# Performance work log

Measured on AMD Instinct MI355X. Metric: run time of the kernel, lower is better.

The kernel has to match this reference:

```python
import jax, jax.numpy as jnp
import numpy as np

B, D_IN, D_OUT, E = 8192, 1024, 1024, 16

def setup_inputs() -> dict:
    key = jax.random.key(0)
    k1, k2, k3 = jax.random.split(key, 3)
    scale_in = 1.0 / np.sqrt(D_IN)
    return {
        "x": jax.random.normal(k1, (B, D_IN), dtype=jnp.float32),
        "Wg": jax.random.normal(k2, (D_IN, E), dtype=jnp.float32) * scale_in,
        "bg": jnp.zeros((E,), dtype=jnp.float32),
        "We": jax.random.normal(k3, (E, D_IN, D_OUT), dtype=jnp.float32) * scale_in,
        "be": jnp.zeros((E, D_OUT), dtype=jnp.float32),
    }

def reference(x, Wg, bg, We, be):
    # gate: Linear + softmax over experts  -> [B, E]
    gate_probs = jax.nn.softmax(x @ Wg + bg, axis=1)
    # all experts as one batched GEMM: [B, E, D_OUT]
    expert_outputs = jnp.einsum("bi,eio->beo", x, We) + be[None, :, :]
    # gate-weighted sum over experts -> [B, D_OUT]
    return jnp.einsum("be,beo->bo", gate_probs, expert_outputs)
```

## Files before the change

### kernel.cpp

```cpp
#include <hip/hip_runtime.h>
#include <hip/hip_bf16.h>

#define NB 8192
#define DIN 1024
#define DOUT 1024
#define NE 16

#define BM 256
#define BN 256
#define BK 64
#define NT 128

typedef __attribute__((ext_vector_type(8))) short bf16x8;
typedef __attribute__((ext_vector_type(4))) short short4_t;
typedef __attribute__((ext_vector_type(4))) float f32x4;

__device__ __forceinline__ unsigned short f32_to_bf16(float f) {
  unsigned int u = __float_as_uint(f);
  u += 0x7FFFu + ((u >> 16) & 1u);
  return (unsigned short)(u >> 16);
}

__device__ __forceinline__ void gl_lds16(const void* gp, void* lp) {
  __builtin_amdgcn_global_load_lds(
      (const __attribute__((address_space(1))) void*)gp,
      (__attribute__((address_space(3))) void*)lp, 16, 0, 0);
}

#define SB __builtin_amdgcn_sched_barrier(0)

__global__ __launch_bounds__(256) void gate_cast_kernel(
    const float* __restrict__ x, const float* __restrict__ Wg,
    const float* __restrict__ bg, float* __restrict__ gout,
    unsigned short* __restrict__ xbf) {
  const int lane = threadIdx.x & 63;
  const int wid = threadIdx.x >> 6;
  const int row = blockIdx.x * 4 + wid;

  const f32x4* xr = (const f32x4*)(x + (size_t)row * DIN);
  f32x4 xv[4];
#pragma unroll
  for (int j = 0; j < 4; ++j) xv[j] = xr[j * 64 + lane];

  float acc[NE];
#pragma unroll
  for (int e = 0; e < NE; ++e) acc[e] = 0.f;

#pragma unroll
  for (int j = 0; j < 4; ++j) {
#pragma unroll
    for (int t = 0; t < 4; ++t) {
      const int i = j * 256 + lane * 4 + t;
      const f32x4* wrow = (const f32x4*)(Wg + (size_t)i * NE);
      const f32x4 w0 = wrow[0], w1 = wrow[1], w2 = wrow[2], w3 = wrow[3];
      const float xx = xv[j][t];
#pragma unroll
      for (int q = 0; q < 4; ++q) {
        acc[q]      = fmaf(xx, w0[q], acc[q]);
        acc[4 + q]  = fmaf(xx, w1[q], acc[4 + q]);
        acc[8 + q]  = fmaf(xx, w2[q], acc[8 + q]);
        acc[12 + q] = fmaf(xx, w3[q], acc[12 + q]);
      }
    }
  }
#pragma unroll
  for (int off = 32; off >= 1; off >>= 1) {
#pragma unroll
    for (int e = 0; e < NE; ++e) acc[e] += __shfl_xor(acc[e], off, 64);
  }
#pragma unroll
  for (int e = 0; e < NE; ++e) acc[e] += bg[e];
  float mx = acc[0];
#pragma unroll
  for (int e = 1; e < NE; ++e) mx = fmaxf(mx, acc[e]);
  float p[NE];
  float s = 0.f;
#pragma unroll
  for (int e = 0; e < NE; ++e) { p[e] = expf(acc[e] - mx); s += p[e]; }
  const float inv = 1.f / s;
  if (lane == 0) {
#pragma unroll
    for (int e = 0; e < NE; ++e) gout[(size_t)row * NE + e] = p[e] * inv;
  }
#pragma unroll
  for (int j = 0; j < 4; ++j) {
    short4_t o;
#pragma unroll
    for (int t = 0; t < 4; ++t) o[t] = (short)f32_to_bf16(xv[j][t]);
    *(short4_t*)(xbf + (size_t)row * DIN + j * 256 + lane * 4) = o;
  }
}

__global__ __launch_bounds__(256) void we_transpose_kernel(
    const float* __restrict__ We, unsigned short* __restrict__ WeT) {
  __shared__ float tile[64][65];
  const int e = blockIdx.z, it = blockIdx.y, ot = blockIdx.x;
  const int tr = threadIdx.x >> 4;
  const int tc = (threadIdx.x & 15) * 4;
  const float* src = We + (((size_t)e * DIN + it * 64) * DOUT) + ot * 64;
#pragma unroll
  for (int rr = 0; rr < 64; rr += 16) {
    const f32x4 v = *(const f32x4*)(src + (size_t)(rr + tr) * DOUT + tc);
#pragma unroll
    for (int t = 0; t < 4; ++t) tile[rr + tr][tc + t] = v[t];
  }
  __syncthreads();
  unsigned short* dst = WeT + (((size_t)e * DOUT + ot * 64) * DIN) + it * 64;
#pragma unroll
  for (int rr = 0; rr < 64; rr += 16) {
    short4_t o;
#pragma unroll
    for (int t = 0; t < 4; ++t) o[t] = (short)f32_to_bf16(tile[tc + t][rr + tr]);
    *(short4_t*)(dst + (size_t)(rr + tr) * DIN + tc) = o;
  }
}

__global__ __launch_bounds__(512, 2) void moe_gemm_kernel(
    const unsigned short* __restrict__ xbf,
    const unsigned short* __restrict__ WeT,
    const float* __restrict__ g,
    const float* __restrict__ be,
    float* __restrict__ out) {
  __shared__ __align__(16) unsigned short As[2][BM * BK];
  __shared__ __align__(16) unsigned short Bs[2][BN * BK];
  __shared__ float gs[BM][NE];

  const int tid = threadIdx.x;
  const int lane = tid & 63, wid = tid >> 6;
  const int wm = wid >> 2, wn = wid & 3;
  const int l15 = lane & 15, l4 = lane >> 4;

  const int bid = blockIdx.x;
  const int xcd = bid & 7, jj_ = bid >> 3;
  const int kh = xcd >> 2;
  const int brow = ((xcd & 3) * 8 + (jj_ >> 2)) * BM;
  const int bcol = (jj_ & 3) * BN;

  const int swz0 = (l4 * 16) ^ ((l15 & 7) << 4);
  const int swz1 = (64 + l4 * 16) ^ ((l15 & 7) << 4);
  const char* const ldsA0 = (const char*)&As[0][0] + (wm * 128 + l15) * 128 + swz0;
  const char* const ldsA1 = (const char*)&As[0][0] + (wm * 128 + l15) * 128 + swz1;
  const char* const ldsB0 = (const char*)&Bs[0][0] + (wn * 64 + l15) * 128 + swz0;
  const char* const ldsB1 = (const char*)&Bs[0][0] + (wn * 64 + l15) * 128 + swz1;

  const int srow = tid >> 3;
  const int lk = (((tid & 7) * 16) ^ ((srow & 7) << 4)) >> 1;
  const unsigned short* const aBase = xbf + (size_t)(brow + srow) * DIN + lk;
  const unsigned short* const bBase = WeT + (size_t)(bcol + srow) * DIN + lk;
  char* const ldsStA = (char*)&As[0][0] + wid * 1024;
  char* const ldsStB = (char*)&Bs[0][0] + wid * 1024;

#define STA(BUF, CR, KC) \
  gl_lds16(aBase + (size_t)(CR) * DIN + (KC), ldsStA + (BUF) * 32768 + (CR) * 128)
#define STB(BUF, CR, EOFF, KC) \
  gl_lds16(bBase + (EOFF) + (size_t)(CR) * DIN + (KC), \
           ldsStB + (BUF) * 32768 + (CR) * 128)
#define RD_B(KS, BUF)                                             \
  _Pragma("unroll") for (int ni = 0; ni < 4; ++ni)                \
      bfr[ni][KS] = *(const bf16x8*)(((KS) ? ldsB1 : ldsB0) +     \
                                     ni * 2048 + (BUF) * 32768);
#define RD_A(KS, MI0, BUF)                                        \
  _Pragma("unroll") for (int d = 0; d < 4; ++d)                   \
      af[d] = *(const bf16x8*)(((KS) ? ldsA1 : ldsA0) +           \
                               ((MI0) + d) * 2048 + (BUF) * 32768);
#define MFMA_P(MI0, KS)                                            \
  _Pragma("unroll") for (int d = 0; d < 4; ++d)                    \
  _Pragma("unroll") for (int ni = 0; ni < 4; ++ni)                 \
      acc[(MI0) + d][ni] = __builtin_amdgcn_mfma_f32_16x16x32_bf16(\
          af[d], bfr[ni][KS], acc[(MI0) + d][ni], 0, 0, 0);

  {
    const f32x4* gsrc = (const f32x4*)(g + (size_t)brow * NE);
    f32x4* gdst = (f32x4*)&gs[0][0];
    gdst[tid] = gsrc[tid];
    gdst[tid + 512] = gsrc[tid + 512];
  }

  {
    const size_t e0 = (size_t)(kh * 8) * (size_t)(DIN * DOUT);
    STB(0, 0, e0, 0);  STB(0, 128, e0, 0);
    STB(0, 64, e0, 0); STB(0, 192, e0, 0);
    STA(0, 0, 0);      STA(0, 128, 0);
    STA(0, 64, 0);     STA(0, 192, 0);
  }

  f32x4 acc[8][4];
#pragma unroll
  for (int mi = 0; mi < 8; ++mi)
#pragma unroll
    for (int ni = 0; ni < 4; ++ni) acc[mi][ni] = (f32x4){0.f, 0.f, 0.f, 0.f};

  asm volatile("s_waitcnt vmcnt(2) lgkmcnt(0)" ::: "memory");
  __builtin_amdgcn_s_barrier(); SB;

  bf16x8 bfr[4][2], af[4];

#define TILE_BODY(T, BUF)                                                      \
  {                                                                            \
    const int t_ = (T);                                                        \
    const int kcN = ((t_ + 1) & 15) * 64;                                      \
    const size_t eoffN =                                                       \
        (size_t)(kh * 8 + ((t_ + 1) >> 4)) * (size_t)(DIN * DOUT);             \
    const bool hasNext = (t_ + 1) < NT;                                        \
    if ((t_ & 15) == 0 && t_ > 0) {               \
      const int e = kh * 8 + (t_ >> 4);                                        \
      _Pragma("unroll") for (int mi = 0; mi < 8; ++mi) {                       \
        const int rb = wm * 128 + mi * 16 + l4 * 4;                            \
        _Pragma("unroll") for (int q = 0; q < 4; ++q) {                        \
          const float r = gs[rb + q][e - 1] *                                  \
                          __builtin_amdgcn_rcpf(fmaxf(gs[rb + q][e], 1e-30f)); \
          _Pragma("unroll") for (int ni = 0; ni < 4; ++ni)                     \
              acc[mi][ni][q] *= r;                                             \
        }                                                                      \
      }                                                                        \
    }                                                                          \
                                           \
    if (hasNext) {                                                             \
      STB(BUF ^ 1, 0, eoffN, kcN); STB(BUF ^ 1, 128, eoffN, kcN);              \
      STB(BUF ^ 1, 64, eoffN, kcN); STB(BUF ^ 1, 192, eoffN, kcN);             \
      STA(BUF ^ 1, 0, kcN); STA(BUF ^ 1, 128, kcN);                            \
    }                                                                          \
    RD_B(0, BUF); RD_B(1, BUF);                                                \
    RD_A(0, 0, BUF);                                                           \
    __builtin_amdgcn_s_setprio(1); MFMA_P(0, 0);                               \
    __builtin_amdgcn_s_setprio(0);                                             \
    RD_A(1, 0, BUF);                                                           \
    __builtin_amdgcn_s_setprio(1); MFMA_P(0, 1);                               \
    __builtin_amdgcn_s_setprio(0);                                             \
    if (hasNext) { asm volatile("s_waitcnt vmcnt(6)" ::: "memory"); }          \
    else         { asm volatile("s_waitcnt vmcnt(0)" ::: "memory"); }          \
    __builtin_amdgcn_s_barrier(); SB;                                          \
                                           \
    if (hasNext) { STA(BUF ^ 1, 64, kcN); STA(BUF ^ 1, 192, kcN); }            \
    RD_A(0, 4, BUF);                                                           \
    __builtin_amdgcn_s_setprio(1); MFMA_P(4, 0);                               \
    __builtin_amdgcn_s_setprio(0);                                             \
    RD_A(1, 4, BUF);                                                           \
    __builtin_amdgcn_s_setprio(1); MFMA_P(4, 1);                               \
    __builtin_amdgcn_s_setprio(0);                                             \
    if (hasNext) { asm volatile("s_waitcnt vmcnt(2)" ::: "memory"); }          \
    __builtin_amdgcn_s_barrier(); SB;                                          \
  }

  for (int tt = 0; tt < NT; tt += 2) {
    TILE_BODY(tt, 0);
    TILE_BODY(tt + 1, 1);
  }

  const int eL = kh * 8 + 7;
  float bv[8][4];
#pragma unroll
  for (int e8 = 0; e8 < 8; ++e8)
#pragma unroll
    for (int ni = 0; ni < 4; ++ni)
      bv[e8][ni] = be[(kh * 8 + e8) * DOUT + bcol + wn * 64 + ni * 16 + l15];
#pragma unroll
  for (int mi = 0; mi < 8; ++mi) {
    const int rb = wm * 128 + mi * 16 + l4 * 4;
#pragma unroll
    for (int q = 0; q < 4; ++q) {
      const int row = rb + q;
      const float gf = gs[row][eL];
      float b0 = 0.f, b1 = 0.f, b2 = 0.f, b3 = 0.f;
#pragma unroll
      for (int e8 = 0; e8 < 8; ++e8) {
        const float ge = gs[row][kh * 8 + e8];
        b0 = fmaf(ge, bv[e8][0], b0);
        b1 = fmaf(ge, bv[e8][1], b1);
        b2 = fmaf(ge, bv[e8][2], b2);
        b3 = fmaf(ge, bv[e8][3], b3);
      }
      float* const orp =
          out + (size_t)(brow + row) * DOUT + bcol + wn * 64 + l15;
      atomicAdd(orp,      fmaf(acc[mi][0][q], gf, b0));
      atomicAdd(orp + 16, fmaf(acc[mi][1][q], gf, b1));
      atomicAdd(orp + 32, fmaf(acc[mi][2][q], gf, b2));
      atomicAdd(orp + 48, fmaf(acc[mi][3][q], gf, b3));
    }
  }
#undef TILE_BODY
#undef MFMA_P
#undef RD_A
#undef RD_B
#undef STA
#undef STB
}

extern "C" void kernel_launch(void* const* d_in, const int* in_sizes, int n_in,
                              void* d_out, int out_size, void* d_ws, size_t ws_size,
                              hipStream_t stream) {
  const float* x  = (const float*)d_in[0];
  const float* Wg = (const float*)d_in[1];
  const float* bg = (const float*)d_in[2];
  const float* We = (const float*)d_in[3];
  const float* be = (const float*)d_in[4];
  float* out = (float*)d_out;

  char* ws = (char*)d_ws;
  unsigned short* xbf = (unsigned short*)ws;
  unsigned short* WeT = (unsigned short*)(ws + (size_t)NB * DIN * 2);
  float* g = (float*)(ws + (size_t)NB * DIN * 2 + (size_t)NE * DIN * DOUT * 2);

  hipMemsetAsync(out, 0, (size_t)NB * DOUT * sizeof(float), stream);
  gate_cast_kernel<<<dim3(NB / 4), 256, 0, stream>>>(x, Wg, bg, g, xbf);
  we_transpose_kernel<<<dim3(DOUT / 64, DIN / 64, NE), 256, 0, stream>>>(We, WeT);
  moe_gemm_kernel<<<dim3(256), 512, 0, stream>>>(xbf, WeT, g, be, out);
}
```

Baseline: 375.4 us.

## Software-pipeline LDS fragment reads with double-buffered A registers across MFMA phases

Restructures the main tile loop so LDS reads for the next MFMA phase are issued ahead of the current MFMA block. Two A-fragment register slots alternate between phases, and the first fragments of the next tile are prefetched after the end-of-tile barrier. Global-to-LDS loads are spread across the four phases, with adjusted waitcnt and barrier placement. It also folds the per-expert bias into the accumulator at each expert boundary. This is meant to hide LDS read latency behind MFMAs, at the cost of extra registers and the risk of subtle ordering bugs or changed bias numerics.

Measured after the change: 365.9 us. 1.03x faster.

```diff
diff --git a/kernel.cpp b/kernel.cpp
--- a/kernel.cpp
+++ b/kernel.cpp
@@ -155,19 +155,19 @@
 #define STB(BUF, CR, EOFF, KC) \
   gl_lds16(bBase + (EOFF) + (size_t)(CR) * DIN + (KC), \
            ldsStB + (BUF) * 32768 + (CR) * 128)
-#define RD_B(KS, BUF)                                             \
+#define ISSUE_B(KS, BUF)                                          \
   _Pragma("unroll") for (int ni = 0; ni < 4; ++ni)                \
       bfr[ni][KS] = *(const bf16x8*)(((KS) ? ldsB1 : ldsB0) +     \
                                      ni * 2048 + (BUF) * 32768);
-#define RD_A(KS, MI0, BUF)                                        \
+#define ISSUE_A(SL, KS, MI0, BUF)                                 \
   _Pragma("unroll") for (int d = 0; d < 4; ++d)                   \
-      af[d] = *(const bf16x8*)(((KS) ? ldsA1 : ldsA0) +           \
+      SL[d] = *(const bf16x8*)(((KS) ? ldsA1 : ldsA0) +           \
                                ((MI0) + d) * 2048 + (BUF) * 32768);
-#define MFMA_P(MI0, KS)                                            \
+#define MFMA_C(MI0, KS, SL)                                        \
   _Pragma("unroll") for (int d = 0; d < 4; ++d)                    \
   _Pragma("unroll") for (int ni = 0; ni < 4; ++ni)                 \
       acc[(MI0) + d][ni] = __builtin_amdgcn_mfma_f32_16x16x32_bf16(\
-          af[d], bfr[ni][KS], acc[(MI0) + d][ni], 0, 0, 0);
+          SL[d], bfr[ni][KS], acc[(MI0) + d][ni], 0, 0, 0);
 
   {
     const f32x4* gsrc = (const f32x4*)(g + (size_t)brow * NE);
@@ -190,10 +190,11 @@
 #pragma unroll
     for (int ni = 0; ni < 4; ++ni) acc[mi][ni] = (f32x4){0.f, 0.f, 0.f, 0.f};
 
+  bf16x8 bfr[4][2], afS0[4], afS1[4];
+
   asm volatile("s_waitcnt vmcnt(2) lgkmcnt(0)" ::: "memory");
   __builtin_amdgcn_s_barrier(); SB;
-
-  bf16x8 bfr[4][2], af[4];
+  ISSUE_B(0, 0); ISSUE_A(afS0, 0, 0, 0);
 
 #define TILE_BODY(T, BUF)                                                      \
   {                                                                            \
@@ -202,8 +203,8 @@
     const size_t eoffN =                                                       \
         (size_t)(kh * 8 + ((t_ + 1) >> 4)) * (size_t)(DIN * DOUT);             \
     const bool hasNext = (t_ + 1) < NT;                                        \
-    if ((t_ & 15) == 0 && t_ > 0) {               \
-      const int e = kh * 8 + (t_ >> 4);                                        \
+    if ((t_ & 15) == 0 && t_ > 0) { \
+      const int e = kh * 8 + (t_ >> 4); \
       _Pragma("unroll") for (int mi = 0; mi < 8; ++mi) {                       \
         const int rb = wm * 128 + mi * 16 + l4 * 4;                            \
         _Pragma("unroll") for (int q = 0; q < 4; ++q) {                        \
@@ -214,32 +215,42 @@
         }                                                                      \
       }                                                                        \
     }                                                                          \
-                                           \
+                   \
+    if (hasNext) { STB(BUF ^ 1, 0, eoffN, kcN); STB(BUF ^ 1, 128, eoffN, kcN); } \
+    ISSUE_B(1, BUF); ISSUE_A(afS1, 1, 0, BUF);                                 \
+    __builtin_amdgcn_s_setprio(1); MFMA_C(0, 0, afS0);                         \
+    __builtin_amdgcn_s_setprio(0);                                             \
+      \
+    if (hasNext) { STB(BUF ^ 1, 64, eoffN, kcN); STB(BUF ^ 1, 192, eoffN, kcN); } \
+    if (t_ == NT - 1) { asm volatile("s_waitcnt vmcnt(0)" ::: "memory"); }     \
+    else { asm volatile("s_waitcnt vmcnt(4)" ::: "memory"); }                  \
+    __builtin_amdgcn_s_barrier(); SB;                                          \
+    ISSUE_A(afS0, 0, 4, BUF);                                                  \
+    __builtin_amdgcn_s_setprio(1); MFMA_C(0, 1, afS1);                         \
+    __builtin_amdgcn_s_setprio(0);                                             \
+                   \
+    if (hasNext) { STA(BUF ^ 1, 0, kcN); STA(BUF ^ 1, 128, kcN); }             \
+    ISSUE_A(afS1, 1, 4, BUF);                                                  \
+    __builtin_amdgcn_s_setprio(1); MFMA_C(4, 0, afS0);                         \
+    __builtin_amdgcn_s_setprio(0);                                             \
+          \
+    if (hasNext) { STA(BUF ^ 1, 64, kcN); STA(BUF ^ 1, 192, kcN); }            \
+    __builtin_amdgcn_s_setprio(1); MFMA_C(4, 1, afS1);                         \
+    __builtin_amdgcn_s_setprio(0);                                             \
+    if ((t_ & 15) == 15) {                              \
+      const int e = kh * 8 + (t_ >> 4);                                        \
+      _Pragma("unroll") for (int ni = 0; ni < 4; ++ni) {                       \
+        const float bv = be[e * DOUT + bcol + wn * 64 + ni * 16 + l15];        \
+        _Pragma("unroll") for (int mi = 0; mi < 8; ++mi)                       \
+          _Pragma("unroll") for (int q = 0; q < 4; ++q)                        \
+              acc[mi][ni][q] += bv;                                            \
+      }                                                                        \
+    }                                                                          \
     if (hasNext) {                                                             \
-      STB(BUF ^ 1, 0, eoffN, kcN); STB(BUF ^ 1, 128, eoffN, kcN);              \
-      STB(BUF ^ 1, 64, eoffN, kcN); STB(BUF ^ 1, 192, eoffN, kcN);             \
-      STA(BUF ^ 1, 0, kcN); STA(BUF ^ 1, 128, kcN);                            \
+      asm volatile("s_waitcnt vmcnt(2)" ::: "memory");                         \
+      __builtin_amdgcn_s_barrier(); SB;                                        \
+      ISSUE_B(0, BUF ^ 1); ISSUE_A(afS0, 0, 0, BUF ^ 1);                       \
     }                                                                          \
-    RD_B(0, BUF); RD_B(1, BUF);                                                \
-    RD_A(0, 0, BUF);                                                           \
-    __builtin_amdgcn_s_setprio(1); MFMA_P(0, 0);                               \
-    __builtin_amdgcn_s_setprio(0);                                             \
-    RD_A(1, 0, BUF);                                                           \
-    __builtin_amdgcn_s_setprio(1); MFMA_P(0, 1);                               \
-    __builtin_amdgcn_s_setprio(0);                                             \
-    if (hasNext) { asm volatile("s_waitcnt vmcnt(6)" ::: "memory"); }          \
-    else         { asm volatile("s_waitcnt vmcnt(0)" ::: "memory"); }          \
-    __builtin_amdgcn_s_barrier(); SB;                                          \
-                                           \
-    if (hasNext) { STA(BUF ^ 1, 64, kcN); STA(BUF ^ 1, 192, kcN); }            \
-    RD_A(0, 4, BUF);                                                           \
-    __builtin_amdgcn_s_setprio(1); MFMA_P(4, 0);                               \
-    __builtin_amdgcn_s_setprio(0);                                             \
-    RD_A(1, 4, BUF);                                                           \
-    __builtin_amdgcn_s_setprio(1); MFMA_P(4, 1);                               \
-    __builtin_amdgcn_s_setprio(0);                                             \
-    if (hasNext) { asm volatile("s_waitcnt vmcnt(2)" ::: "memory"); }          \
-    __builtin_amdgcn_s_barrier(); SB;                                          \
   }
 
   for (int tt = 0; tt < NT; tt += 2) {
@@ -279,9 +290,9 @@
     }
   }
 #undef TILE_BODY
-#undef MFMA_P
-#undef RD_A
-#undef RD_B
+#undef MFMA_C
+#undef ISSUE_A
+#undef ISSUE_B
 #undef STA
 #undef STB
 }
```

## Switch GEMM mainloop to 4-stage BK=32 pipeline with in-loop bias add

Applied to the files above, without the earlier changes.

Halves the K tile to 32 and uses a four-buffer LDS ring that prefetches three tiles ahead instead of double buffering, with a new swizzle and staging layout for 64-byte rows. Global-to-LDS loads are interleaved with the MFMA halves and guarded by vmcnt waits sized for the deeper pipeline. Bias for each expert is now added into the accumulators at the end of that expert's K range, rather than in the epilogue. This is meant to hide memory latency better, at the cost of twice as many barriers per unit of K work and a different LDS access pattern. The epilogue shown before still adds bias, so bias may be applied twice unless the hidden part was changed.

Result: no change. 380.8 us (+1.4%).

```diff
diff --git a/kernel.cpp b/kernel.cpp
--- a/kernel.cpp
+++ b/kernel.cpp
@@ -8,8 +8,8 @@
 
 #define BM 256
 #define BN 256
-#define BK 64
-#define NT 128
+#define BK 32
+#define NT 256
 
 typedef __attribute__((ext_vector_type(8))) short bf16x8;
 typedef __attribute__((ext_vector_type(4))) short short4_t;
@@ -121,8 +121,8 @@
     const float* __restrict__ g,
     const float* __restrict__ be,
     float* __restrict__ out) {
-  __shared__ __align__(16) unsigned short As[2][BM * BK];
-  __shared__ __align__(16) unsigned short Bs[2][BN * BK];
+  __shared__ __align__(16) unsigned short As[4][BM * BK];
+  __shared__ __align__(16) unsigned short Bs[4][BN * BK];
   __shared__ float gs[BM][NE];
 
   const int tid = threadIdx.x;
@@ -136,38 +136,33 @@
   const int brow = ((xcd & 3) * 8 + (jj_ >> 2)) * BM;
   const int bcol = (jj_ & 3) * BN;
 
-  const int swz0 = (l4 * 16) ^ ((l15 & 7) << 4);
-  const int swz1 = (64 + l4 * 16) ^ ((l15 & 7) << 4);
-  const char* const ldsA0 = (const char*)&As[0][0] + (wm * 128 + l15) * 128 + swz0;
-  const char* const ldsA1 = (const char*)&As[0][0] + (wm * 128 + l15) * 128 + swz1;
-  const char* const ldsB0 = (const char*)&Bs[0][0] + (wn * 64 + l15) * 128 + swz0;
-  const char* const ldsB1 = (const char*)&Bs[0][0] + (wn * 64 + l15) * 128 + swz1;
-
-  const int srow = tid >> 3;
-  const int lk = (((tid & 7) * 16) ^ ((srow & 7) << 4)) >> 1;
+  const int rswz = ((l4 ^ (l15 & 3)) << 4);
+  const char* const ldsA = (const char*)&As[0][0] + (wm * 128 + l15) * 64 + rswz;
+  const char* const ldsB = (const char*)&Bs[0][0] + (wn * 64 + l15) * 64 + rswz;
+
+  const int srow = tid >> 2;
+  const int lk = ((((tid & 3) << 4) ^ ((srow & 3) << 4)) >> 1);
   const unsigned short* const aBase = xbf + (size_t)(brow + srow) * DIN + lk;
   const unsigned short* const bBase = WeT + (size_t)(bcol + srow) * DIN + lk;
   char* const ldsStA = (char*)&As[0][0] + wid * 1024;
   char* const ldsStB = (char*)&Bs[0][0] + wid * 1024;
 
 #define STA(BUF, CR, KC) \
-  gl_lds16(aBase + (size_t)(CR) * DIN + (KC), ldsStA + (BUF) * 32768 + (CR) * 128)
+  gl_lds16(aBase + (size_t)(CR) * DIN + (KC), ldsStA + (BUF) * 16384 + (CR) * 64)
 #define STB(BUF, CR, EOFF, KC) \
   gl_lds16(bBase + (EOFF) + (size_t)(CR) * DIN + (KC), \
-           ldsStB + (BUF) * 32768 + (CR) * 128)
-#define RD_B(KS, BUF)                                             \
-  _Pragma("unroll") for (int ni = 0; ni < 4; ++ni)                \
-      bfr[ni][KS] = *(const bf16x8*)(((KS) ? ldsB1 : ldsB0) +     \
-                                     ni * 2048 + (BUF) * 32768);
-#define RD_A(KS, MI0, BUF)                                        \
-  _Pragma("unroll") for (int d = 0; d < 4; ++d)                   \
-      af[d] = *(const bf16x8*)(((KS) ? ldsA1 : ldsA0) +           \
-                               ((MI0) + d) * 2048 + (BUF) * 32768);
-#define MFMA_P(MI0, KS)                                            \
+           ldsStB + (BUF) * 16384 + (CR) * 64)
+#define RD_B(BUF)                                                  \
+  _Pragma("unroll") for (int ni = 0; ni < 4; ++ni)                 \
+      bfr[ni] = *(const bf16x8*)(ldsB + ni * 1024 + (BUF) * 16384);
+#define RD_A(MI0, BUF)                                             \
+  _Pragma("unroll") for (int d = 0; d < 4; ++d)                    \
+      af[d] = *(const bf16x8*)(ldsA + ((MI0) + d) * 1024 + (BUF) * 16384);
+#define MFMA_P(MI0)                                                \
   _Pragma("unroll") for (int d = 0; d < 4; ++d)                    \
   _Pragma("unroll") for (int ni = 0; ni < 4; ++ni)                 \
       acc[(MI0) + d][ni] = __builtin_amdgcn_mfma_f32_16x16x32_bf16(\
-          af[d], bfr[ni][KS], acc[(MI0) + d][ni], 0, 0, 0);
+          af[d], bfr[ni], acc[(MI0) + d][ni], 0, 0, 0);
 
   {
     const f32x4* gsrc = (const f32x4*)(g + (size_t)brow * NE);
@@ -178,10 +173,9 @@
 
   {
     const size_t e0 = (size_t)(kh * 8) * (size_t)(DIN * DOUT);
-    STB(0, 0, e0, 0);  STB(0, 128, e0, 0);
-    STB(0, 64, e0, 0); STB(0, 192, e0, 0);
-    STA(0, 0, 0);      STA(0, 128, 0);
-    STA(0, 64, 0);     STA(0, 192, 0);
+    STB(0, 0, e0, 0);  STB(0, 128, e0, 0);  STA(0, 0, 0);  STA(0, 128, 0);
+    STB(1, 0, e0, 32); STB(1, 128, e0, 32); STA(1, 0, 32); STA(1, 128, 32);
+    STB(2, 0, e0, 64); STB(2, 128, e0, 64); STA(2, 0, 64); STA(2, 128, 64);
   }
 
   f32x4 acc[8][4];
@@ -190,20 +184,22 @@
 #pragma unroll
     for (int ni = 0; ni < 4; ++ni) acc[mi][ni] = (f32x4){0.f, 0.f, 0.f, 0.f};
 
-  asm volatile("s_waitcnt vmcnt(2) lgkmcnt(0)" ::: "memory");
+  asm volatile("s_waitcnt vmcnt(8) lgkmcnt(0)" ::: "memory");
   __builtin_amdgcn_s_barrier(); SB;
 
-  bf16x8 bfr[4][2], af[4];
+  bf16x8 bfr[4], af[4];
 
 #define TILE_BODY(T, BUF)                                                      \
   {                                                                            \
     const int t_ = (T);                                                        \
-    const int kcN = ((t_ + 1) & 15) * 64;                                      \
-    const size_t eoffN =                                                       \
-        (size_t)(kh * 8 + ((t_ + 1) >> 4)) * (size_t)(DIN * DOUT);             \
-    const bool hasNext = (t_ + 1) < NT;                                        \
-    if ((t_ & 15) == 0 && t_ > 0) {               \
-      const int e = kh * 8 + (t_ >> 4);                                        \
+    const int sT = t_ + 3;                                                     \
+    const bool doStage = sT < NT;                                              \
+    const int bufS = ((BUF) + 3) & 3;                                          \
+    const int kcS = (sT & 31) * 32;                                            \
+    const size_t eoffS =                                                       \
+        (size_t)(kh * 8 + (sT >> 5)) * (size_t)(DIN * DOUT);                   \
+    if ((t_ & 31) == 0 && t_ > 0) {               \
+      const int e = kh * 8 + (t_ >> 5);                                        \
       _Pragma("unroll") for (int mi = 0; mi < 8; ++mi) {                       \
         const int rb = wm * 128 + mi * 16 + l4 * 4;                            \
         _Pragma("unroll") for (int q = 0; q < 4; ++q) {                        \
@@ -214,37 +210,39 @@
         }                                                                      \
       }                                                                        \
     }                                                                          \
-                                           \
-    if (hasNext) {                                                             \
-      STB(BUF ^ 1, 0, eoffN, kcN); STB(BUF ^ 1, 128, eoffN, kcN);              \
-      STB(BUF ^ 1, 64, eoffN, kcN); STB(BUF ^ 1, 192, eoffN, kcN);             \
-      STA(BUF ^ 1, 0, kcN); STA(BUF ^ 1, 128, kcN);                            \
+                                                    \
+    RD_B(BUF); RD_A(0, BUF);                                                   \
+    if (doStage) { STB(bufS, 0, eoffS, kcS); STB(bufS, 128, eoffS, kcS); }     \
+    __builtin_amdgcn_s_barrier(); SB;                                          \
+    __builtin_amdgcn_s_setprio(1); MFMA_P(0);                                  \
+    __builtin_amdgcn_s_setprio(0);                                             \
+                                                    \
+    RD_A(4, BUF);                                                              \
+    if (doStage) { STA(bufS, 0, kcS); STA(bufS, 128, kcS); }                   \
+    __builtin_amdgcn_s_barrier(); SB;                                          \
+    __builtin_amdgcn_s_setprio(1); MFMA_P(4);                                  \
+    __builtin_amdgcn_s_setprio(0);                                             \
+    if ((t_ & 31) == 31) {                              \
+      const int e = kh * 8 + (t_ >> 5);                                        \
+      _Pragma("unroll") for (int ni = 0; ni < 4; ++ni) {                       \
+        const float bv = be[e * DOUT + bcol + wn * 64 + ni * 16 + l15];        \
+        _Pragma("unroll") for (int mi = 0; mi < 8; ++mi)                       \
+          _Pragma("unroll") for (int q = 0; q < 4; ++q)                        \
+              acc[mi][ni][q] += bv;                                            \
+      }                                                                        \
     }                                                                          \
-    RD_B(0, BUF); RD_B(1, BUF);                                                \
-    RD_A(0, 0, BUF);                                                           \
-    __builtin_amdgcn_s_setprio(1); MFMA_P(0, 0);                               \
-    __builtin_amdgcn_s_setprio(0);                                             \
-    RD_A(1, 0, BUF);                                                           \
-    __builtin_amdgcn_s_setprio(1); MFMA_P(0, 1);                               \
-    __builtin_amdgcn_s_setprio(0);                                             \
-    if (hasNext) { asm volatile("s_waitcnt vmcnt(6)" ::: "memory"); }          \
-    else         { asm volatile("s_waitcnt vmcnt(0)" ::: "memory"); }          \
-    __builtin_amdgcn_s_barrier(); SB;                                          \
-                                           \
-    if (hasNext) { STA(BUF ^ 1, 64, kcN); STA(BUF ^ 1, 192, kcN); }            \
-    RD_A(0, 4, BUF);                                                           \
-    __builtin_amdgcn_s_setprio(1); MFMA_P(4, 0);                               \
-    __builtin_amdgcn_s_setprio(0);                                             \
-    RD_A(1, 4, BUF);                                                           \
-    __builtin_amdgcn_s_setprio(1); MFMA_P(4, 1);                               \
-    __builtin_amdgcn_s_setprio(0);                                             \
-    if (hasNext) { asm volatile("s_waitcnt vmcnt(2)" ::: "memory"); }          \
-    __builtin_amdgcn_s_barrier(); SB;                                          \
-  }
-
-  for (int tt = 0; tt < NT; tt += 2) {
+                            \
+    if (t_ < NT - 3) { asm volatile("s_waitcnt vmcnt(8)" ::: "memory"); }      \
+    else if (t_ == NT - 3) { asm volatile("s_waitcnt vmcnt(4)" ::: "memory"); }\
+    else if (t_ == NT - 2) { asm volatile("s_waitcnt vmcnt(0)" ::: "memory"); }\
+    if (t_ < NT - 1) { __builtin_amdgcn_s_barrier(); SB; }                     \
+  }
+
+  for (int tt = 0; tt < NT; tt += 4) {
     TILE_BODY(tt, 0);
     TILE_BODY(tt + 1, 1);
+    TILE_BODY(tt + 2, 2);
+    TILE_BODY(tt + 3, 3);
   }
 
   const int eL = kh * 8 + 7;
```
